# Kernel tuning notes

Measured on AMD Instinct MI355X. Metric: run time of the kernel, lower is better.

## Reference

```python
import jax, jax.numpy as jnp
import numpy as np

B, C, X = 64, 2, 262144
H = 256          # hidden_dim
K = 8            # max_fronts
THR = 1e-06      # diff_threshold
LN_EPS = 1e-5


def _layernorm(x, g, b):
    mu = jnp.mean(x, axis=-1, keepdims=True)
    var = jnp.var(x, axis=-1, keepdims=True)
    return (x - mu) * jax.lax.rsqrt(var + LN_EPS) * g + b


def setup_inputs() -> dict:
    key = jax.random.key(0)
    ks = jax.random.split(key, 16)
    density = jax.random.normal(ks[0], (B, X), dtype=jnp.float32)
    coords = jnp.broadcast_to(jnp.linspace(0.0, 1.0, X, dtype=jnp.float32), (B, X))
    x = jnp.stack([density, coords], axis=1)  # (B, 2, X)

    def lin(k, fan_in, shape):
        return jax.random.normal(k, shape, dtype=jnp.float32) * (1.0 / np.sqrt(fan_in))

    inp = {
        "x": x,
        # input_proj: Linear(6, H) + LayerNorm(H)
        "w_in": lin(ks[1], 6, (6, H)),
        "b_in": jnp.zeros((H,), jnp.float32),
        "ln_in_g": jnp.ones((H,), jnp.float32),
        "ln_in_b": jnp.zeros((H,), jnp.float32),
        # 3 residual blocks, stacked on leading axis
        "rb_ln_g": jnp.ones((3, H), jnp.float32),
        "rb_ln_b": jnp.zeros((3, H), jnp.float32),
        "rb_w1": lin(ks[2], H, (3, H, 2 * H)),
        "rb_b1": jnp.zeros((3, 2 * H), jnp.float32),
        "rb_w2": lin(ks[3], 2 * H, (3, 2 * H, H)),
        "rb_b2": jnp.zeros((3, H), jnp.float32),
        # output head: LayerNorm(H) -> Linear(H, H//2) -> GELU -> Linear(H//2, 2)
        "out_ln_g": jnp.ones((H,), jnp.float32),
        "out_ln_b": jnp.zeros((H,), jnp.float32),
        "out_w1": lin(ks[4], H, (H, H // 2)),
        "out_b1": jnp.zeros((H // 2,), jnp.float32),
        "out_w2": lin(ks[5], H // 2, (H // 2, 2)),
        "out_b2": jnp.zeros((2,), jnp.float32),
    }
    return inp


def _speed_predictor(uL, uR, w_in, b_in, ln_in_g, ln_in_b,
                     rb_ln_g, rb_ln_b, rb_w1, rb_b1, rb_w2, rb_b2,
                     out_ln_g, out_ln_b, out_w1, out_b1, out_w2, out_b2):
    diff = uL - uR
    feats = jnp.stack([uL, uR, diff, jnp.abs(diff), (uL + uR) * 0.5,
                       jnp.sign(diff)], axis=-1)          # (B, K, 6)
    h = jax.nn.gelu(_layernorm(feats @ w_in + b_in, ln_in_g, ln_in_b),
                    approximate=False)                    # (B, K, H)
    for i in range(3):  # fixed small layer loop
        z = _layernorm(h, rb_ln_g[i], rb_ln_b[i])
        z = jax.nn.gelu(z @ rb_w1[i] + rb_b1[i], approximate=False)
        h = h + (z @ rb_w2[i] + rb_b2[i])
    z = _layernorm(h, out_ln_g, out_ln_b)
    z = jax.nn.gelu(z @ out_w1 + out_b1, approximate=False)
    return z @ out_w2 + out_b2                            # (B, K, 2)


def reference(x, w_in, b_in, ln_in_g, ln_in_b,
              rb_ln_g, rb_ln_b, rb_w1, rb_b1, rb_w2, rb_b2,
              out_ln_g, out_ln_b, out_w1, out_b1, out_w2, out_b2):
    density = x[:, 0, :]
    coords = x[:, -1, :]
    left_vals, right_vals = density[:, :-1], density[:, 1:]
    has_disc = jnp.abs(left_vals - right_vals) > THR       # (B, X-1)
    all_fc = (coords[:, :-1] + coords[:, 1:]) * 0.5        # (B, X-1)
    front_count = jnp.sum(has_disc, axis=-1)               # (B,)
    score = jnp.where(has_disc, all_fc, jnp.inf)
    # smallest-K coords -> top_k of negated score (K <= X-1 here)
    _, idx = jax.lax.top_k(-score, K)                      # (B, K)
    uL = jnp.take_along_axis(left_vals, idx, axis=-1)
    uR = jnp.take_along_axis(right_vals, idx, axis=-1)
    fc = jnp.take_along_axis(all_fc, idx, axis=-1)
    valid = jnp.take_along_axis(has_disc, idx, axis=-1).astype(x.dtype)
    speed = _speed_predictor(uL, uR, w_in, b_in, ln_in_g, ln_in_b,
                             rb_ln_g, rb_ln_b, rb_w1, rb_b1, rb_w2, rb_b2,
                             out_ln_g, out_ln_b, out_w1, out_b1, out_w2, out_b2)
    front_params = jnp.concatenate(
        [jnp.transpose(speed, (0, 2, 1)),                  # (B, 2, K)
         uL[:, None], uR[:, None], fc[:, None], valid[:, None]], axis=1)
    return front_params, front_count
```

## Files before the change

### kernel.cpp

```cpp
#include <hip/hip_runtime.h>
#include <hip/hip_bf16.h>
#include <math.h>

#define XN 262144
#define NPAIR (XN - 1)
#define BN 64
#define HD 256
#define KK 8
#define THRC 1e-6f

__device__ __forceinline__ float gelu_f(float x) {
    return 0.5f * x * (1.0f + erff(x * 0.70710678118654752440f));
}

__global__ __launch_bounds__(64) void select_kernel(const float* __restrict__ x,
                                                    float* __restrict__ out,
                                                    float* __restrict__ ws_uLuR) {
    const int b = blockIdx.x;
    const float* d = x + (size_t)b * 2 * XN;
    const float* c = d + XN;
    const int lane = threadIdx.x;

    int idxs[KK];
    float vflag[KK];
    int found = 0;

    for (int base = 0; base < NPAIR && found < KK; base += 64) {
        int i = base + lane;
        bool v = (i < NPAIR) && (fabsf(d[i] - d[i + 1]) > THRC);
        unsigned long long m = __ballot(v);
        while (m && found < KK) {
            int l = __ffsll(m) - 1;
            idxs[found] = base + l;
            vflag[found] = 1.0f;
            ++found;
            m &= (m - 1);
        }
    }
    if (found < KK) {
        for (int base = 0; base < NPAIR && found < KK; base += 64) {
            int i = base + lane;
            bool v = (i < NPAIR) && !(fabsf(d[i] - d[i + 1]) > THRC);
            unsigned long long m = __ballot(v);
            while (m && found < KK) {
                int l = __ffsll(m) - 1;
                idxs[found] = base + l;
                vflag[found] = 0.0f;
                ++found;
                m &= (m - 1);
            }
        }
    }

    if (lane < KK) {
        int i = idxs[lane];
        float uL = d[i];
        float uR = d[i + 1];
        float fc = (c[i] + c[i + 1]) * 0.5f;
        float* o = out + b * 48;
        o[16 + lane] = uL;
        o[24 + lane] = uR;
        o[32 + lane] = fc;
        o[40 + lane] = vflag[lane];
        ws_uLuR[(b * KK + lane) * 2 + 0] = uL;
        ws_uLuR[(b * KK + lane) * 2 + 1] = uR;
    }
}

__global__ __launch_bounds__(256) void count_kernel(const float* __restrict__ x,
                                                    int* __restrict__ ws_cnt) {
    __shared__ int sred[4];
    const int b = blockIdx.x >> 5;
    const int p = blockIdx.x & 31;
    const float* row = x + (size_t)b * 2 * XN;
    const int tid = threadIdx.x;

    int cnt = 0;
    const int base0 = p * 8192;
#pragma unroll
    for (int it = 0; it < 8; ++it) {
        int e0 = base0 + ((it << 8) + tid) * 4;
        float4 f = *(const float4*)(row + e0);
        cnt += (fabsf(f.x - f.y) > THRC);
        cnt += (fabsf(f.y - f.z) > THRC);
        cnt += (fabsf(f.z - f.w) > THRC);
        if (e0 + 4 < XN) {
            float e = row[e0 + 4];
            cnt += (fabsf(f.w - e) > THRC);
        }
    }
#pragma unroll
    for (int off = 32; off > 0; off >>= 1) cnt += __shfl_down(cnt, off, 64);
    int lane = tid & 63, wave = tid >> 6;
    if (lane == 0) sred[wave] = cnt;
    __syncthreads();
    if (tid == 0) ws_cnt[b * 32 + p] = sred[0] + sred[1] + sred[2] + sred[3];
}


#define FMA4(acc, w4, zc)                    \
    acc.x = fmaf(w4.x, zc, acc.x);           \
    acc.y = fmaf(w4.y, zc, acc.y);           \
    acc.z = fmaf(w4.z, zc, acc.z);           \
    acc.w = fmaf(w4.w, zc, acc.w);

__global__ __launch_bounds__(512) void mlp_kernel(
    const float* __restrict__ ws_uLuR, const int* __restrict__ ws_cnt,
    const float* __restrict__ w_in, const float* __restrict__ b_in,
    const float* __restrict__ ln_in_g, const float* __restrict__ ln_in_b,
    const float* __restrict__ rb_ln_g, const float* __restrict__ rb_ln_b,
    const float* __restrict__ rb_w1, const float* __restrict__ rb_b1,
    const float* __restrict__ rb_w2, const float* __restrict__ rb_b2,
    const float* __restrict__ out_ln_g, const float* __restrict__ out_ln_b,
    const float* __restrict__ out_w1, const float* __restrict__ out_b1,
    const float* __restrict__ out_w2, const float* __restrict__ out_b2,
    float* __restrict__ out) {
    __shared__ float4 hsv[HD];
    __shared__ float4 ztv[HD];
    __shared__ float4 z2tv[2 * HD];
    __shared__ float4 z3tv[HD / 2];
    __shared__ float part[8192];
    __shared__ float red[4][4][2];
    __shared__ float stat[4][2];
    __shared__ float fin[2][8];

    const int tid = threadIdx.x;
    const int bid = blockIdx.x;
    const int b = bid >> 1;
    const int half = bid & 1;

    if (half == 0 && tid == 0) {
        int s = 0;
        for (int p = 0; p < 32; ++p) s += ws_cnt[b * 32 + p];
        out[3072 + b] = (float)s;
    }

    const int wave = tid >> 6, lane = tid & 63;

    if (tid < HD) {
        const int c = tid;
        float fw[6];
#pragma unroll
        for (int f = 0; f < 6; ++f) fw[f] = w_in[f * HD + c];
        float bin = b_in[c];
        float4 hv;
        float* hvp = (float*)&hv;
#pragma unroll
        for (int j = 0; j < 4; ++j) {
            int tok = b * KK + half * 4 + j;
            float uL = ws_uLuR[tok * 2 + 0];
            float uR = ws_uLuR[tok * 2 + 1];
            float dd = uL - uR;
            float sg = (dd > 0.0f) ? 1.0f : ((dd < 0.0f) ? -1.0f : 0.0f);
            hvp[j] = bin + uL * fw[0] + uR * fw[1] + dd * fw[2] +
                     fabsf(dd) * fw[3] + (uL + uR) * 0.5f * fw[4] + sg * fw[5];
        }
        hsv[c] = hv;
    }
    __syncthreads();

#define LN_STATS()                                                            \
    do {                                                                      \
        if (tid < HD) {                                                       \
            float4 h4 = hsv[tid];                                             \
            float s[4] = {h4.x, h4.y, h4.z, h4.w};                            \
            float q[4] = {h4.x * h4.x, h4.y * h4.y, h4.z * h4.z, h4.w * h4.w};\
            for (int off = 32; off > 0; off >>= 1) {                          \
                _Pragma("unroll") for (int j = 0; j < 4; ++j) {               \
                    s[j] += __shfl_down(s[j], off, 64);                       \
                    q[j] += __shfl_down(q[j], off, 64);                       \
                }                                                             \
            }                                                                 \
            if (lane == 0) {                                                  \
                _Pragma("unroll") for (int j = 0; j < 4; ++j) {               \
                    red[wave][j][0] = s[j];                                   \
                    red[wave][j][1] = q[j];                                   \
                }                                                             \
            }                                                                 \
        }                                                                     \
        __syncthreads();                                                      \
        if (tid < 4) {                                                        \
            float ts = 0.0f, tq = 0.0f;                                       \
            _Pragma("unroll") for (int w = 0; w < 4; ++w) {                   \
                ts += red[w][tid][0];                                         \
                tq += red[w][tid][1];                                         \
            }                                                                 \
            float mu = ts * (1.0f / 256.0f);                                  \
            float vr = tq * (1.0f / 256.0f) - mu * mu;                        \
            stat[tid][0] = mu;                                                \
            stat[tid][1] = rsqrtf(vr + 1e-5f);                                \
        }                                                                     \
        __syncthreads();                                                      \
    } while (0)

    LN_STATS();
    if (tid < HD) {
        const int c = tid;
        float g = ln_in_g[c], be = ln_in_b[c];
        float4 hv = hsv[c];
        float* hvp = (float*)&hv;
#pragma unroll
        for (int j = 0; j < 4; ++j)
            hvp[j] = gelu_f((hvp[j] - stat[j][0]) * stat[j][1] * g + be);
        hsv[c] = hv;
    }
    __syncthreads();

    for (int i = 0; i < 3; ++i) {
        LN_STATS();
        if (tid < HD) {
            const int c = tid;
            float gg = rb_ln_g[i * HD + c], bb = rb_ln_b[i * HD + c];
            float4 hv = hsv[c], zv;
            float* hvp = (float*)&hv;
            float* zvp = (float*)&zv;
#pragma unroll
            for (int j = 0; j < 4; ++j)
                zvp[j] = (hvp[j] - stat[j][0]) * stat[j][1] * gg + bb;
            ztv[c] = zv;
        }
        __syncthreads();

        {
            const float* w1 = rb_w1 + (size_t)i * HD * 2 * HD;
            const int cg = tid & 127, kh = tid >> 7;
            const float* wp = w1 + (size_t)(kh * 64) * (2 * HD) + cg * 4;
            float4 a0 = {0, 0, 0, 0}, a1 = {0, 0, 0, 0}, a2 = {0, 0, 0, 0},
                   a3 = {0, 0, 0, 0};
#pragma unroll 8
            for (int k = 0; k < 64; ++k) {
                float4 w4 = *(const float4*)wp;
                wp += 2 * HD;
                float4 z4 = ztv[kh * 64 + k];
                FMA4(a0, w4, z4.x);
                FMA4(a1, w4, z4.y);
                FMA4(a2, w4, z4.z);
                FMA4(a3, w4, z4.w);
            }
            float* pp = part + (kh * 128 + cg) * 16;
            *(float4*)(pp + 0) = a0;
            *(float4*)(pp + 4) = a1;
            *(float4*)(pp + 8) = a2;
            *(float4*)(pp + 12) = a3;
        }
        __syncthreads();
        {
            const int c2 = tid;
            const int cg = c2 >> 2, c = c2 & 3;
            float b1v = rb_b1[i * 2 * HD + c2];
            float4 zv;
            float* zvp = (float*)&zv;
#pragma unroll
            for (int j = 0; j < 4; ++j) {
                int o = cg * 16 + j * 4 + c;
                float v = b1v + part[o] + part[o + 2048] + part[o + 4096] +
                          part[o + 6144];
                zvp[j] = gelu_f(v);
            }
            z2tv[c2] = zv;
        }
        __syncthreads();

        {
            const float* w2 = rb_w2 + (size_t)i * 2 * HD * HD;
            const int cg2 = tid & 63, kh2 = tid >> 6;
            const float* wp = w2 + (size_t)(kh2 * 64) * HD + cg2 * 4;
            float4 a0 = {0, 0, 0, 0}, a1 = {0, 0, 0, 0}, a2 = {0, 0, 0, 0},
                   a3 = {0, 0, 0, 0};
#pragma unroll 8
            for (int k = 0; k < 64; ++k) {
                float4 w4 = *(const float4*)wp;
                wp += HD;
                float4 z4 = z2tv[kh2 * 64 + k];
                FMA4(a0, w4, z4.x);
                FMA4(a1, w4, z4.y);
                FMA4(a2, w4, z4.z);
                FMA4(a3, w4, z4.w);
            }
            float* pp = part + (kh2 * 64 + cg2) * 16;
            *(float4*)(pp + 0) = a0;
            *(float4*)(pp + 4) = a1;
            *(float4*)(pp + 8) = a2;
            *(float4*)(pp + 12) = a3;
        }
        __syncthreads();
        if (tid < HD) {
            const int c2 = tid;
            const int cg2 = c2 >> 2, c = c2 & 3;
            float b2v = rb_b2[i * HD + c2];
            float4 hv = hsv[c2];
            float* hvp = (float*)&hv;
#pragma unroll
            for (int j = 0; j < 4; ++j) {
                int o = cg2 * 16 + j * 4 + c;
                float v = b2v;
#pragma unroll
                for (int kh = 0; kh < 8; ++kh) v += part[o + kh * 1024];
                hvp[j] += v;
            }
            hsv[c2] = hv;
        }
        __syncthreads();
    }

    LN_STATS();
    if (tid < HD) {
        const int c = tid;
        float gg = out_ln_g[c], bb = out_ln_b[c];
        float4 hv = hsv[c], zv;
        float* hvp = (float*)&hv;
        float* zvp = (float*)&zv;
#pragma unroll
        for (int j = 0; j < 4; ++j)
            zvp[j] = (hvp[j] - stat[j][0]) * stat[j][1] * gg + bb;
        ztv[c] = zv;
    }
    __syncthreads();

    {
        const int cg3 = tid & 31, kh3 = tid >> 5;
        const float* wp = out_w1 + (size_t)(kh3 * 16) * (HD / 2) + cg3 * 4;
        float4 a0 = {0, 0, 0, 0}, a1 = {0, 0, 0, 0}, a2 = {0, 0, 0, 0},
               a3 = {0, 0, 0, 0};
#pragma unroll 4
        for (int k = 0; k < 16; ++k) {
            float4 w4 = *(const float4*)wp;
            wp += HD / 2;
            float4 z4 = ztv[kh3 * 16 + k];
            FMA4(a0, w4, z4.x);
            FMA4(a1, w4, z4.y);
            FMA4(a2, w4, z4.z);
            FMA4(a3, w4, z4.w);
        }
        float* pp = part + (kh3 * 32 + cg3) * 16;
        *(float4*)(pp + 0) = a0;
        *(float4*)(pp + 4) = a1;
        *(float4*)(pp + 8) = a2;
        *(float4*)(pp + 12) = a3;
    }
    __syncthreads();
    if (tid < HD / 2) {
        const int c2 = tid;
        const int cg3 = c2 >> 2, c = c2 & 3;
        float bv = out_b1[c2];
        float4 zv;
        float* zvp = (float*)&zv;
#pragma unroll
        for (int j = 0; j < 4; ++j) {
            int o = cg3 * 16 + j * 4 + c;
            float v = bv;
#pragma unroll
            for (int kh = 0; kh < 16; ++kh) v += part[o + kh * 512];
            zvp[j] = gelu_f(v);
        }
        z3tv[c2] = zv;
    }
    __syncthreads();

    if (tid < HD / 2) {
        float4 z = z3tv[tid];
        float w0 = out_w2[tid * 2 + 0];
        float w1v = out_w2[tid * 2 + 1];
        float p[8];
        p[0] = z.x * w0; p[1] = z.x * w1v;
        p[2] = z.y * w0; p[3] = z.y * w1v;
        p[4] = z.z * w0; p[5] = z.z * w1v;
        p[6] = z.w * w0; p[7] = z.w * w1v;
#pragma unroll
        for (int off = 32; off > 0; off >>= 1) {
#pragma unroll
            for (int u = 0; u < 8; ++u) p[u] += __shfl_down(p[u], off, 64);
        }
        if (lane == 0) {
#pragma unroll
            for (int u = 0; u < 8; ++u) fin[wave][u] = p[u];
        }
    }
    __syncthreads();
    if (tid < 8) {
        int j = tid >> 1;
        int o = tid & 1;
        float s = out_b2[o] + fin[0][tid] + fin[1][tid];
        out[b * 48 + o * 8 + half * 4 + j] = s;
    }
}

extern "C" void kernel_launch(void* const* d_in, const int* in_sizes, int n_in,
                              void* d_out, int out_size, void* d_ws, size_t ws_size,
                              hipStream_t stream) {
    const float* x        = (const float*)d_in[0];
    const float* w_in     = (const float*)d_in[1];
    const float* b_in     = (const float*)d_in[2];
    const float* ln_in_g  = (const float*)d_in[3];
    const float* ln_in_b  = (const float*)d_in[4];
    const float* rb_ln_g  = (const float*)d_in[5];
    const float* rb_ln_b  = (const float*)d_in[6];
    const float* rb_w1    = (const float*)d_in[7];
    const float* rb_b1    = (const float*)d_in[8];
    const float* rb_w2    = (const float*)d_in[9];
    const float* rb_b2    = (const float*)d_in[10];
    const float* out_ln_g = (const float*)d_in[11];
    const float* out_ln_b = (const float*)d_in[12];
    const float* out_w1   = (const float*)d_in[13];
    const float* out_b1   = (const float*)d_in[14];
    const float* out_w2   = (const float*)d_in[15];
    const float* out_b2   = (const float*)d_in[16];

    float* out = (float*)d_out;
    float* wsf = (float*)d_ws;
    int* wsc = (int*)(wsf + 1024);

    select_kernel<<<BN, 64, 0, stream>>>(x, out, wsf);
    count_kernel<<<BN * 32, 256, 0, stream>>>(x, wsc);
    mlp_kernel<<<BN * 2, 512, 0, stream>>>(
        wsf, wsc, w_in, b_in, ln_in_g, ln_in_b, rb_ln_g, rb_ln_b,
        rb_w1, rb_b1, rb_w2, rb_b2, out_ln_g, out_ln_b,
        out_w1, out_b1, out_w2, out_b2, out);
}
```

Before: 270.8 us.

## Fuse select into count kernel and split MLP tokens across four blocks

Merges the front-selection kernel into the counting kernel, so one launch handles both. The counting blocks now cover twice as many elements each (16 per batch instead of 32). The MLP kernel now processes 2 tokens per block instead of 4, doubling the grid to 256 blocks to spread the weight-streaming GEMV work across more CUs. The trade-off is that each weight matrix is reread by twice as many blocks and there is less register reuse per weight load. The selection work now sits inside one block of the count grid and may lengthen that block.

```diff
diff --git a/kernel.cpp b/kernel.cpp
--- a/kernel.cpp
+++ b/kernel.cpp
@@ -13,72 +13,66 @@
     return 0.5f * x * (1.0f + erff(x * 0.70710678118654752440f));
 }
 
-__global__ __launch_bounds__(64) void select_kernel(const float* __restrict__ x,
-                                                    float* __restrict__ out,
-                                                    float* __restrict__ ws_uLuR) {
-    const int b = blockIdx.x;
-    const float* d = x + (size_t)b * 2 * XN;
-    const float* c = d + XN;
-    const int lane = threadIdx.x;
-
-    int idxs[KK];
-    float vflag[KK];
-    int found = 0;
-
-    for (int base = 0; base < NPAIR && found < KK; base += 64) {
-        int i = base + lane;
-        bool v = (i < NPAIR) && (fabsf(d[i] - d[i + 1]) > THRC);
-        unsigned long long m = __ballot(v);
-        while (m && found < KK) {
-            int l = __ffsll(m) - 1;
-            idxs[found] = base + l;
-            vflag[found] = 1.0f;
-            ++found;
-            m &= (m - 1);
-        }
-    }
-    if (found < KK) {
+__global__ __launch_bounds__(256) void count_select_kernel(
+    const float* __restrict__ x, float* __restrict__ out,
+    float* __restrict__ ws_uLuR, int* __restrict__ ws_cnt) {
+    __shared__ int sred[4];
+    const int b = blockIdx.x >> 4;
+    const int p = blockIdx.x & 15;
+    const float* row = x + (size_t)b * 2 * XN;
+    const int tid = threadIdx.x;
+    const int lane = tid & 63, wave = tid >> 6;
+
+    if (p == 0 && tid < 64) {
+        const float* c = row + XN;
+        int idxs[KK];
+        float vflag[KK];
+        int found = 0;
         for (int base = 0; base < NPAIR && found < KK; base += 64) {
             int i = base + lane;
-            bool v = (i < NPAIR) && !(fabsf(d[i] - d[i + 1]) > THRC);
+            bool v = (i < NPAIR) && (fabsf(row[i] - row[i + 1]) > THRC);
             unsigned long long m = __ballot(v);
             while (m && found < KK) {
                 int l = __ffsll(m) - 1;
                 idxs[found] = base + l;
-                vflag[found] = 0.0f;
+                vflag[found] = 1.0f;
                 ++found;
                 m &= (m - 1);
             }
         }
-    }
-
-    if (lane < KK) {
-        int i = idxs[lane];
-        float uL = d[i];
-        float uR = d[i + 1];
-        float fc = (c[i] + c[i + 1]) * 0.5f;
-        float* o = out + b * 48;
-        o[16 + lane] = uL;
-        o[24 + lane] = uR;
-        o[32 + lane] = fc;
-        o[40 + lane] = vflag[lane];
-        ws_uLuR[(b * KK + lane) * 2 + 0] = uL;
-        ws_uLuR[(b * KK + lane) * 2 + 1] = uR;
-    }
-}
-
-__global__ __launch_bounds__(256) void count_kernel(const float* __restrict__ x,
-                                                    int* __restrict__ ws_cnt) {
-    __shared__ int sred[4];
-    const int b = blockIdx.x >> 5;
-    const int p = blockIdx.x & 31;
-    const float* row = x + (size_t)b * 2 * XN;
-    const int tid = threadIdx.x;
+        if (found < KK) {
+            for (int base = 0; base < NPAIR && found < KK; base += 64) {
+                int i = base + lane;
+                bool v = (i < NPAIR) && !(fabsf(row[i] - row[i + 1]) > THRC);
+                unsigned long long m = __ballot(v);
+                while (m && found < KK) {
+                    int l = __ffsll(m) - 1;
+                    idxs[found] = base + l;
+                    vflag[found] = 0.0f;
+                    ++found;
+                    m &= (m - 1);
+                }
+            }
+        }
+        if (lane < KK) {
+            int i = idxs[lane];
+            float uL = row[i];
+            float uR = row[i + 1];
+            float fc = (c[i] + c[i + 1]) * 0.5f;
+            float* o = out + b * 48;
+            o[16 + lane] = uL;
+            o[24 + lane] = uR;
+            o[32 + lane] = fc;
+            o[40 + lane] = vflag[lane];
+            ws_uLuR[(b * KK + lane) * 2 + 0] = uL;
+            ws_uLuR[(b * KK + lane) * 2 + 1] = uR;
+        }
+    }
 
     int cnt = 0;
-    const int base0 = p * 8192;
-#pragma unroll
-    for (int it = 0; it < 8; ++it) {
+    const int base0 = p * 16384;
+#pragma unroll
+    for (int it = 0; it < 16; ++it) {
         int e0 = base0 + ((it << 8) + tid) * 4;
         float4 f = *(const float4*)(row + e0);
         cnt += (fabsf(f.x - f.y) > THRC);
@@ -91,18 +85,21 @@
     }
 #pragma unroll
     for (int off = 32; off > 0; off >>= 1) cnt += __shfl_down(cnt, off, 64);
-    int lane = tid & 63, wave = tid >> 6;
     if (lane == 0) sred[wave] = cnt;
     __syncthreads();
-    if (tid == 0) ws_cnt[b * 32 + p] = sred[0] + sred[1] + sred[2] + sred[3];
+    if (tid == 0) ws_cnt[blockIdx.x] = sred[0] + sred[1] + sred[2] + sred[3];
 }
 
 
-#define FMA4(acc, w4, zc)                    \
-    acc.x = fmaf(w4.x, zc, acc.x);           \
-    acc.y = fmaf(w4.y, zc, acc.y);           \
-    acc.z = fmaf(w4.z, zc, acc.z);           \
-    acc.w = fmaf(w4.w, zc, acc.w);
+#define FMA4x2(a0, a1, w4, z2v)              \
+    a0.x = fmaf(w4.x, z2v.x, a0.x);          \
+    a0.y = fmaf(w4.y, z2v.x, a0.y);          \
+    a0.z = fmaf(w4.z, z2v.x, a0.z);          \
+    a0.w = fmaf(w4.w, z2v.x, a0.w);          \
+    a1.x = fmaf(w4.x, z2v.y, a1.x);          \
+    a1.y = fmaf(w4.y, z2v.y, a1.y);          \
+    a1.z = fmaf(w4.z, z2v.y, a1.z);          \
+    a1.w = fmaf(w4.w, z2v.y, a1.w);
 
 __global__ __launch_bounds__(512) void mlp_kernel(
     const float* __restrict__ ws_uLuR, const int* __restrict__ ws_cnt,
@@ -115,27 +112,27 @@
     const float* __restrict__ out_w1, const float* __restrict__ out_b1,
     const float* __restrict__ out_w2, const float* __restrict__ out_b2,
     float* __restrict__ out) {
-    __shared__ float4 hsv[HD];
-    __shared__ float4 ztv[HD];
-    __shared__ float4 z2tv[2 * HD];
-    __shared__ float4 z3tv[HD / 2];
-    __shared__ float part[8192];
-    __shared__ float red[4][4][2];
-    __shared__ float stat[4][2];
-    __shared__ float fin[2][8];
+    __shared__ float2 hsv[HD];
+    __shared__ float2 ztv[HD];
+    __shared__ float2 z2tv[2 * HD];
+    __shared__ float2 z3tv[HD / 2];
+    __shared__ float part[4096];
+    __shared__ float red[8][2][2];
+    __shared__ float stat[2][2];
+    __shared__ float fin[2][4];
 
     const int tid = threadIdx.x;
     const int bid = blockIdx.x;
-    const int b = bid >> 1;
-    const int half = bid & 1;
-
-    if (half == 0 && tid == 0) {
-        int s = 0;
-        for (int p = 0; p < 32; ++p) s += ws_cnt[b * 32 + p];
-        out[3072 + b] = (float)s;
-    }
-
+    const int b = bid >> 2;
+    const int sub = bid & 3;
     const int wave = tid >> 6, lane = tid & 63;
+
+    if (sub == 0 && wave == 0) {
+        int v = (lane < 16) ? ws_cnt[b * 16 + lane] : 0;
+#pragma unroll
+        for (int off = 8; off > 0; off >>= 1) v += __shfl_down(v, off, 64);
+        if (lane == 0) out[3072 + b] = (float)v;
+    }
 
     if (tid < HD) {
         const int c = tid;
@@ -143,11 +140,11 @@
 #pragma unroll
         for (int f = 0; f < 6; ++f) fw[f] = w_in[f * HD + c];
         float bin = b_in[c];
-        float4 hv;
+        float2 hv;
         float* hvp = (float*)&hv;
 #pragma unroll
-        for (int j = 0; j < 4; ++j) {
-            int tok = b * KK + half * 4 + j;
+        for (int j = 0; j < 2; ++j) {
+            int tok = b * KK + sub * 2 + j;
             float uL = ws_uLuR[tok * 2 + 0];
             float uR = ws_uLuR[tok * 2 + 1];
             float dd = uL - uR;
@@ -162,24 +159,24 @@
 #define LN_STATS()                                                            \
     do {                                                                      \
         if (tid < HD) {                                                       \
-            float4 h4 = hsv[tid];                                             \
-            float s[4] = {h4.x, h4.y, h4.z, h4.w};                            \
-            float q[4] = {h4.x * h4.x, h4.y * h4.y, h4.z * h4.z, h4.w * h4.w};\
+            float2 h2 = hsv[tid];                                             \
+            float s[2] = {h2.x, h2.y};                                        \
+            float q[2] = {h2.x * h2.x, h2.y * h2.y};                          \
             for (int off = 32; off > 0; off >>= 1) {                          \
-                _Pragma("unroll") for (int j = 0; j < 4; ++j) {               \
+                _Pragma("unroll") for (int j = 0; j < 2; ++j) {               \
                     s[j] += __shfl_down(s[j], off, 64);                       \
                     q[j] += __shfl_down(q[j], off, 64);                       \
                 }                                                             \
             }                                                                 \
             if (lane == 0) {                                                  \
-                _Pragma("unroll") for (int j = 0; j < 4; ++j) {               \
+                _Pragma("unroll") for (int j = 0; j < 2; ++j) {               \
                     red[wave][j][0] = s[j];                                   \
                     red[wave][j][1] = q[j];                                   \
                 }                                                             \
             }                                                                 \
         }                                                                     \
         __syncthreads();                                                      \
-        if (tid < 4) {                                                        \
+        if (tid < 2) {                                                        \
             float ts = 0.0f, tq = 0.0f;                                       \
             _Pragma("unroll") for (int w = 0; w < 4; ++w) {                   \
                 ts += red[w][tid][0];                                         \
@@ -197,11 +194,9 @@
     if (tid < HD) {
         const int c = tid;
         float g = ln_in_g[c], be = ln_in_b[c];
-        float4 hv = hsv[c];
-        float* hvp = (float*)&hv;
-#pragma unroll
-        for (int j = 0; j < 4; ++j)
-            hvp[j] = gelu_f((hvp[j] - stat[j][0]) * stat[j][1] * g + be);
+        float2 hv = hsv[c];
+        hv.x = gelu_f((hv.x - stat[0][0]) * stat[0][1] * g + be);
+        hv.y = gelu_f((hv.y - stat[1][0]) * stat[1][1] * g + be);
         hsv[c] = hv;
     }
     __syncthreads();
@@ -211,12 +206,9 @@
         if (tid < HD) {
             const int c = tid;
             float gg = rb_ln_g[i * HD + c], bb = rb_ln_b[i * HD + c];
-            float4 hv = hsv[c], zv;
-            float* hvp = (float*)&hv;
-            float* zvp = (float*)&zv;
-#pragma unroll
-            for (int j = 0; j < 4; ++j)
-                zvp[j] = (hvp[j] - stat[j][0]) * stat[j][1] * gg + bb;
+            float2 hv = hsv[c], zv;
+            zv.x = (hv.x - stat[0][0]) * stat[0][1] * gg + bb;
+            zv.y = (hv.y - stat[1][0]) * stat[1][1] * gg + bb;
             ztv[c] = zv;
         }
         __syncthreads();
@@ -225,37 +217,30 @@
             const float* w1 = rb_w1 + (size_t)i * HD * 2 * HD;
             const int cg = tid & 127, kh = tid >> 7;
             const float* wp = w1 + (size_t)(kh * 64) * (2 * HD) + cg * 4;
-            float4 a0 = {0, 0, 0, 0}, a1 = {0, 0, 0, 0}, a2 = {0, 0, 0, 0},
-                   a3 = {0, 0, 0, 0};
+            float4 a0 = {0, 0, 0, 0}, a1 = {0, 0, 0, 0};
 #pragma unroll 8
             for (int k = 0; k < 64; ++k) {
                 float4 w4 = *(const float4*)wp;
                 wp += 2 * HD;
-                float4 z4 = ztv[kh * 64 + k];
-                FMA4(a0, w4, z4.x);
-                FMA4(a1, w4, z4.y);
-                FMA4(a2, w4, z4.z);
-                FMA4(a3, w4, z4.w);
-            }
-            float* pp = part + (kh * 128 + cg) * 16;
+                float2 z2v = ztv[kh * 64 + k];
+                FMA4x2(a0, a1, w4, z2v);
+            }
+            float* pp = part + (kh * 128 + cg) * 8;
             *(float4*)(pp + 0) = a0;
             *(float4*)(pp + 4) = a1;
-            *(float4*)(pp + 8) = a2;
-            *(float4*)(pp + 12) = a3;
         }
         __syncthreads();
         {
             const int c2 = tid;
             const int cg = c2 >> 2, c = c2 & 3;
             float b1v = rb_b1[i * 2 * HD + c2];
-            float4 zv;
-            float* zvp = (float*)&zv;
-#pragma unroll
-            for (int j = 0; j < 4; ++j) {
-                int o = cg * 16 + j * 4 + c;
-                float v = b1v + part[o] + part[o + 2048] + part[o + 4096] +
-                          part[o + 6144];
-                zvp[j] = gelu_f(v);
+            float2 zv;
+#pragma unroll
+            for (int j = 0; j < 2; ++j) {
+                int o = cg * 8 + j * 4 + c;
+                float v = b1v + part[o] + part[o + 1024] + part[o + 2048] +
+                          part[o + 3072];
+                ((float*)&zv)[j] = gelu_f(v);
             }
             z2tv[c2] = zv;
         }
@@ -265,38 +250,31 @@
             const float* w2 = rb_w2 + (size_t)i * 2 * HD * HD;
             const int cg2 = tid & 63, kh2 = tid >> 6;
             const float* wp = w2 + (size_t)(kh2 * 64) * HD + cg2 * 4;
-            float4 a0 = {0, 0, 0, 0}, a1 = {0, 0, 0, 0}, a2 = {0, 0, 0, 0},
-                   a3 = {0, 0, 0, 0};
+            float4 a0 = {0, 0, 0, 0}, a1 = {0, 0, 0, 0};
 #pragma unroll 8
             for (int k = 0; k < 64; ++k) {
                 float4 w4 = *(const float4*)wp;
                 wp += HD;
-                float4 z4 = z2tv[kh2 * 64 + k];
-                FMA4(a0, w4, z4.x);
-                FMA4(a1, w4, z4.y);
-                FMA4(a2, w4, z4.z);
-                FMA4(a3, w4, z4.w);
-            }
-            float* pp = part + (kh2 * 64 + cg2) * 16;
+                float2 z2v = z2tv[kh2 * 64 + k];
+                FMA4x2(a0, a1, w4, z2v);
+            }
+            float* pp = part + (kh2 * 64 + cg2) * 8;
             *(float4*)(pp + 0) = a0;
             *(float4*)(pp + 4) = a1;
-            *(float4*)(pp + 8) = a2;
-            *(float4*)(pp + 12) = a3;
         }
         __syncthreads();
         if (tid < HD) {
             const int c2 = tid;
             const int cg2 = c2 >> 2, c = c2 & 3;
             float b2v = rb_b2[i * HD + c2];
-            float4 hv = hsv[c2];
-            float* hvp = (float*)&hv;
-#pragma unroll
-            for (int j = 0; j < 4; ++j) {
-                int o = cg2 * 16 + j * 4 + c;
+            float2 hv = hsv[c2];
+#pragma unroll
+            for (int j = 0; j < 2; ++j) {
+                int o = cg2 * 8 + j * 4 + c;
                 float v = b2v;
 #pragma unroll
-                for (int kh = 0; kh < 8; ++kh) v += part[o + kh * 1024];
-                hvp[j] += v;
+                for (int kh = 0; kh < 8; ++kh) v += part[o + kh * 512];
+                ((float*)&hv)[j] += v;
             }
             hsv[c2] = hv;
         }
@@ -307,12 +285,9 @@
     if (tid < HD) {
         const int c = tid;
         float gg = out_ln_g[c], bb = out_ln_b[c];
-        float4 hv = hsv[c], zv;
-        float* hvp = (float*)&hv;
-        float* zvp = (float*)&zv;
-#pragma unroll
-        for (int j = 0; j < 4; ++j)
-            zvp[j] = (hvp[j] - stat[j][0]) * stat[j][1] * gg + bb;
+        float2 hv = hsv[c], zv;
+        zv.x = (hv.x - stat[0][0]) * stat[0][1] * gg + bb;
+        zv.y = (hv.y - stat[1][0]) * stat[1][1] * gg + bb;
         ztv[c] = zv;
     }
     __syncthreads();
@@ -320,68 +295,59 @@
     {
         const int cg3 = tid & 31, kh3 = tid >> 5;
         const float* wp = out_w1 + (size_t)(kh3 * 16) * (HD / 2) + cg3 * 4;
-        float4 a0 = {0, 0, 0, 0}, a1 = {0, 0, 0, 0}, a2 = {0, 0, 0, 0},
-               a3 = {0, 0, 0, 0};
+        float4 a0 = {0, 0, 0, 0}, a1 = {0, 0, 0, 0};
 #pragma unroll 4
         for (int k = 0; k < 16; ++k) {
             float4 w4 = *(const float4*)wp;
             wp += HD / 2;
-            float4 z4 = ztv[kh3 * 16 + k];
-            FMA4(a0, w4, z4.x);
-            FMA4(a1, w4, z4.y);
-            FMA4(a2, w4, z4.z);
-            FMA4(a3, w4, z4.w);
-        }
-        float* pp = part + (kh3 * 32 + cg3) * 16;
+            float2 z2v = ztv[kh3 * 16 + k];
+            FMA4x2(a0, a1, w4, z2v);
+        }
+        float* pp = part + (kh3 * 32 + cg3) * 8;
         *(float4*)(pp + 0) = a0;
         *(float4*)(pp + 4) = a1;
-        *(float4*)(pp + 8) = a2;
-        *(float4*)(pp + 12) = a3;
     }
     __syncthreads();
     if (tid < HD / 2) {
         const int c2 = tid;
         const int cg3 = c2 >> 2, c = c2 & 3;
         float bv = out_b1[c2];
-        float4 zv;
-        float* zvp = (float*)&zv;
-#pragma unroll
-        for (int j = 0; j < 4; ++j) {
-            int o = cg3 * 16 + j * 4 + c;
+        float2 zv;
+#pragma unroll
+        for (int j = 0; j < 2; ++j) {
+            int o = cg3 * 8 + j * 4 + c;
             float v = bv;
 #pragma unroll
-            for (int kh = 0; kh < 16; ++kh) v += part[o + kh * 512];
-            zvp[j] = gelu_f(v);
+            for (int kh = 0; kh < 16; ++kh) v += part[o + kh * 256];
+            ((float*)&zv)[j] = gelu_f(v);
         }
         z3tv[c2] = zv;
     }
     __syncthreads();
 
     if (tid < HD / 2) {
-        float4 z = z3tv[tid];
+        float2 z = z3tv[tid];
         float w0 = out_w2[tid * 2 + 0];
         float w1v = out_w2[tid * 2 + 1];
-        float p[8];
+        float p[4];
         p[0] = z.x * w0; p[1] = z.x * w1v;
         p[2] = z.y * w0; p[3] = z.y * w1v;
-        p[4] = z.z * w0; p[5] = z.z * w1v;
-        p[6] = z.w * w0; p[7] = z.w * w1v;
 #pragma unroll
         for (int off = 32; off > 0; off >>= 1) {
 #pragma unroll
-            for (int u = 0; u < 8; ++u) p[u] += __shfl_down(p[u], off, 64);
+            for (int u = 0; u < 4; ++u) p[u] += __shfl_down(p[u], off, 64);
         }
         if (lane == 0) {
 #pragma unroll
-            for (int u = 0; u < 8; ++u) fin[wave][u] = p[u];
-        }
-    }
-    __syncthreads();
-    if (tid < 8) {
+            for (int u = 0; u < 4; ++u) fin[wave][u] = p[u];
+        }
+    }
+    __syncthreads();
+    if (tid < 4) {
         int j = tid >> 1;
         int o = tid & 1;
         float s = out_b2[o] + fin[0][tid] + fin[1][tid];
-        out[b * 48 + o * 8 + half * 4 + j] = s;
+        out[b * 48 + o * 8 + sub * 2 + j] = s;
     }
 }
 
@@ -410,9 +376,8 @@
     float* wsf = (float*)d_ws;
     int* wsc = (int*)(wsf + 1024);
 
-    select_kernel<<<BN, 64, 0, stream>>>(x, out, wsf);
-    count_kernel<<<BN * 32, 256, 0, stream>>>(x, wsc);
-    mlp_kernel<<<BN * 2, 512, 0, stream>>>(
+    count_select_kernel<<<BN * 16, 256, 0, stream>>>(x, out, wsf, wsc);
+    mlp_kernel<<<BN * 4, 512, 0, stream>>>(
         wsf, wsc, w_in, b_in, ln_in_g, ln_in_b, rb_ln_g, rb_ln_b,
         rb_w1, rb_b1, rb_w2, rb_b2, out_ln_g, out_ln_b,
         out_w1, out_b1, out_w2, out_b2, out);
```

Result: faster. 260.1 us (-3.9%).
